# Kernel tuning notes

Measured on AMD Instinct MI355X. Metric: run time of the kernel, lower is better.

Reference implementation:

```python
import jax, jax.numpy as jnp
import numpy as np

N_PIXELS = 1024 * 1024      # flattened image W*H
N_CLASSES = 100             # logit channels / label vocabulary
N_SEGMENTS = 30             # superpixel_regions


def setup_inputs() -> dict:
    key = jax.random.key(0)
    k1, k2, k3 = jax.random.split(key, 3)
    output = jax.random.normal(k1, (N_PIXELS, N_CLASSES), dtype=jnp.float32)
    target = jax.random.randint(k2, (N_PIXELS,), 0, N_CLASSES, dtype=jnp.int64)
    seg_ids = jax.random.randint(k3, (N_PIXELS,), 0, N_SEGMENTS, dtype=jnp.int32)
    return {"output": output, "target": target, "seg_ids": seg_ids}


def reference(output, target, seg_ids):
    # --- per-superpixel histogram mode-voting relabel ---
    # counts[s, c] = number of pixels in superpixel s currently labeled c.
    counts = jnp.zeros((N_SEGMENTS, N_CLASSES), dtype=jnp.int32)
    counts = counts.at[seg_ids, target].add(1)
    # np.argmax over hist of np.unique-sorted labels == smallest class id among ties,
    # which jnp.argmax over the dense class axis reproduces exactly.
    mode = jnp.argmax(counts, axis=1)              # [S]
    relabeled = mode[seg_ids].astype(target.dtype)  # [N]

    # --- CrossEntropyLoss(output, target): mean NLL of log-softmax ---
    logp = jax.nn.log_softmax(output, axis=-1)                       # [N, C]
    nll = -jnp.take_along_axis(logp, target[:, None], axis=-1)[:, 0]  # [N]
    loss = jnp.mean(nll)
    return loss, relabeled
```

## Files before the change

### kernel.cpp

```cpp
#include <hip/hip_runtime.h>
#include <math.h>

#define NCLASS 100
#define NSEG 30

__global__ __launch_bounds__(256) void ce_hist_kernel(
    const float* __restrict__ logits,
    const int*   __restrict__ target,
    const int*   __restrict__ seg,
    int N,
    int*    __restrict__ g_counts,
    double* __restrict__ g_loss)
{
    __shared__ int    lds_hist[NSEG * NCLASS];
    __shared__ double lds_loss[4];

    for (int i = threadIdx.x; i < NSEG * NCLASS; i += blockDim.x) lds_hist[i] = 0;
    __syncthreads();

    const int lane          = threadIdx.x & 63;
    const int wave          = threadIdx.x >> 6;
    const int sub           = lane & 3;
    const int q             = lane >> 2;
    const int wavesPerBlock = blockDim.x >> 6;
    const int gwave         = blockIdx.x * wavesPerBlock + wave;
    const int totWaves      = gridDim.x * wavesPerBlock;
    const int ngroups       = (N + 15) >> 4;

    double acc = 0.0;

    for (int grp = gwave; grp < ngroups; grp += totWaves) {
        const int  row   = grp * 16 + q;
        const bool valid = (row < N);

        const float NEG = -INFINITY;
        float4 f0, f1, f2, f3, f4, f5, f6;
        f0 = f1 = f2 = f3 = f4 = f5 = f6 = make_float4(NEG, NEG, NEG, NEG);
        int t = 0, s = 0;
        float xt = 0.0f;

        if (valid) {
            const float4* r4 = (const float4*)(logits + (size_t)row * NCLASS);
            f0 = r4[sub +  0];
            f1 = r4[sub +  4];
            f2 = r4[sub +  8];
            f3 = r4[sub + 12];
            f4 = r4[sub + 16];
            f5 = r4[sub + 20];
            if (sub == 0) f6 = r4[24];
            t = target[row];
            s = seg[row];
            xt = logits[(size_t)row * NCLASS + t];
        }

        float e = 0.0f;
        e += __expf(f0.x) + __expf(f0.y) + __expf(f0.z) + __expf(f0.w);
        e += __expf(f1.x) + __expf(f1.y) + __expf(f1.z) + __expf(f1.w);
        e += __expf(f2.x) + __expf(f2.y) + __expf(f2.z) + __expf(f2.w);
        e += __expf(f3.x) + __expf(f3.y) + __expf(f3.z) + __expf(f3.w);
        e += __expf(f4.x) + __expf(f4.y) + __expf(f4.z) + __expf(f4.w);
        e += __expf(f5.x) + __expf(f5.y) + __expf(f5.z) + __expf(f5.w);
        e += __expf(f6.x) + __expf(f6.y) + __expf(f6.z) + __expf(f6.w);
        e += __shfl_xor(e, 1);
        e += __shfl_xor(e, 2);

        if (valid && sub == 0) {
            float lse = __logf(e);
            acc += (double)(lse - xt);
            atomicAdd(&lds_hist[s * NCLASS + t], 1);
        }
    }

    #pragma unroll
    for (int off = 32; off; off >>= 1) acc += __shfl_xor(acc, off);
    if (lane == 0) lds_loss[wave] = acc;
    __syncthreads();

    if (threadIdx.x == 0) {
        double b = 0.0;
        for (int w = 0; w < wavesPerBlock; ++w) b += lds_loss[w];
        atomicAdd(g_loss, b);
    }
    for (int i = threadIdx.x; i < NSEG * NCLASS; i += blockDim.x) {
        int c = lds_hist[i];
        if (c) atomicAdd(&g_counts[i], c);
    }
}

__global__ void finalize_kernel(
    const int* __restrict__ g_counts,
    const double* __restrict__ g_loss,
    int N,
    int* __restrict__ g_mode,
    float* __restrict__ out_loss)
{
    const int t = threadIdx.x;
    const int s = t >> 3;
    const int j = t & 7;
    if (s < NSEG) {
        int bestKey = -1;
        #pragma unroll
        for (int c = j; c < NCLASS; c += 8) {
            int v = g_counts[s * NCLASS + c];
            int key = (v << 7) | (127 - c);
            bestKey = max(bestKey, key);
        }
        bestKey = max(bestKey, __shfl_xor(bestKey, 1));
        bestKey = max(bestKey, __shfl_xor(bestKey, 2));
        bestKey = max(bestKey, __shfl_xor(bestKey, 4));
        if (j == 0) g_mode[s] = 127 - (bestKey & 127);
    }
    if (t == 0) out_loss[0] = (float)(g_loss[0] / (double)N);
}

__global__ __launch_bounds__(256) void relabel_kernel(
    const int* __restrict__ seg,
    const int* __restrict__ g_mode,
    float* __restrict__ out,
    int N)
{
    __shared__ float mode_f[NSEG];
    for (int i = threadIdx.x; i < NSEG; i += blockDim.x)
        mode_f[i] = (float)g_mode[i];
    __syncthreads();

    int idx    = blockIdx.x * blockDim.x + threadIdx.x;
    int stride = gridDim.x * blockDim.x;
    for (int i = idx; i < N; i += stride)
        out[i] = mode_f[seg[i]];
}

extern "C" void kernel_launch(void* const* d_in, const int* in_sizes, int n_in,
                              void* d_out, int out_size, void* d_ws, size_t ws_size,
                              hipStream_t stream)
{
    const float* logits = (const float*)d_in[0];
    const int*   target = (const int*)d_in[1];
    const int*   seg    = (const int*)d_in[2];
    float* out = (float*)d_out;

    const int N = in_sizes[1];

    double* g_loss   = (double*)d_ws;
    int*    g_counts = (int*)((char*)d_ws + 16);
    int*    g_mode   = (int*)((char*)d_ws + 16 + NSEG * NCLASS * sizeof(int));

    hipMemsetAsync(d_ws, 0, 16 + NSEG * NCLASS * sizeof(int), stream);

    ce_hist_kernel<<<2048, 256, 0, stream>>>(logits, target, seg, N, g_counts, g_loss);
    finalize_kernel<<<1, 256, 0, stream>>>(g_counts, g_loss, N, g_mode, out);
    relabel_kernel<<<1024, 256, 0, stream>>>(seg, g_mode, out + 1, N);
}
```

Baseline: 117.0 us.

## Coalesce logits loads across 16-row group and reduce partial exps through LDS

Each wave now reads its 16-row group (400 float4s) as one contiguous block with lane-strided float4 loads, instead of per-row strided loads. Per-float4 exp sums are written to a per-wave LDS buffer and regathered per row before the shuffle reduction. The tail-row guard is dropped, so N must be a multiple of 16, and the main grid is halved. The aim is better global memory coalescing, paid for with extra LDS traffic and no intra-wave barrier around the LDS buffer reuse.

```diff
diff --git a/kernel.cpp b/kernel.cpp
--- a/kernel.cpp
+++ b/kernel.cpp
@@ -3,6 +3,13 @@
 
 #define NCLASS 100
 #define NSEG 30
+#define F4_PER_ROW 25
+#define ROWS_PER_GRP 16
+#define F4_PER_GRP (F4_PER_ROW * ROWS_PER_GRP)
+
+__device__ __forceinline__ float e4(float4 v) {
+    return __expf(v.x) + __expf(v.y) + __expf(v.z) + __expf(v.w);
+}
 
 __global__ __launch_bounds__(256) void ce_hist_kernel(
     const float* __restrict__ logits,
@@ -13,67 +20,66 @@
     double* __restrict__ g_loss)
 {
     __shared__ int    lds_hist[NSEG * NCLASS];
+    __shared__ float  part[4][F4_PER_GRP];
     __shared__ double lds_loss[4];
 
     for (int i = threadIdx.x; i < NSEG * NCLASS; i += blockDim.x) lds_hist[i] = 0;
     __syncthreads();
 
     const int lane          = threadIdx.x & 63;
-    const int wave          = threadIdx.x >> 6;
+    const int wv            = threadIdx.x >> 6;
     const int sub           = lane & 3;
     const int q             = lane >> 2;
     const int wavesPerBlock = blockDim.x >> 6;
-    const int gwave         = blockIdx.x * wavesPerBlock + wave;
+    const int gwave         = blockIdx.x * wavesPerBlock + wv;
     const int totWaves      = gridDim.x * wavesPerBlock;
-    const int ngroups       = (N + 15) >> 4;
+    const int ngroups       = N >> 4;
 
     double acc = 0.0;
 
     for (int grp = gwave; grp < ngroups; grp += totWaves) {
-        const int  row   = grp * 16 + q;
-        const bool valid = (row < N);
+        const int row = grp * ROWS_PER_GRP + q;
 
-        const float NEG = -INFINITY;
-        float4 f0, f1, f2, f3, f4, f5, f6;
-        f0 = f1 = f2 = f3 = f4 = f5 = f6 = make_float4(NEG, NEG, NEG, NEG);
-        int t = 0, s = 0;
-        float xt = 0.0f;
+        const int t = target[row];
+        const int s = seg[row];
 
-        if (valid) {
-            const float4* r4 = (const float4*)(logits + (size_t)row * NCLASS);
-            f0 = r4[sub +  0];
-            f1 = r4[sub +  4];
-            f2 = r4[sub +  8];
-            f3 = r4[sub + 12];
-            f4 = r4[sub + 16];
-            f5 = r4[sub + 20];
-            if (sub == 0) f6 = r4[24];
-            t = target[row];
-            s = seg[row];
-            xt = logits[(size_t)row * NCLASS + t];
+        const float4* g4 = (const float4*)logits + (size_t)grp * F4_PER_GRP;
+        float4 f0 = g4[lane        ];
+        float4 f1 = g4[lane + 64   ];
+        float4 f2 = g4[lane + 128  ];
+        float4 f3 = g4[lane + 192  ];
+        float4 f4v= g4[lane + 256  ];
+        float4 f5 = g4[lane + 320  ];
+
+        part[wv][lane      ] = e4(f0);
+        part[wv][lane + 64 ] = e4(f1);
+        part[wv][lane + 128] = e4(f2);
+        part[wv][lane + 192] = e4(f3);
+        part[wv][lane + 256] = e4(f4v);
+        part[wv][lane + 320] = e4(f5);
+        if (lane < 16) {
+            float4 f6 = g4[lane + 384];
+            part[wv][lane + 384] = e4(f6);
         }
 
-        float e = 0.0f;
-        e += __expf(f0.x) + __expf(f0.y) + __expf(f0.z) + __expf(f0.w);
-        e += __expf(f1.x) + __expf(f1.y) + __expf(f1.z) + __expf(f1.w);
-        e += __expf(f2.x) + __expf(f2.y) + __expf(f2.z) + __expf(f2.w);
-        e += __expf(f3.x) + __expf(f3.y) + __expf(f3.z) + __expf(f3.w);
-        e += __expf(f4.x) + __expf(f4.y) + __expf(f4.z) + __expf(f4.w);
-        e += __expf(f5.x) + __expf(f5.y) + __expf(f5.z) + __expf(f5.w);
-        e += __expf(f6.x) + __expf(f6.y) + __expf(f6.z) + __expf(f6.w);
+        const int base = F4_PER_ROW * q + sub;
+        float e = part[wv][base     ] + part[wv][base + 4 ] + part[wv][base + 8 ]
+                + part[wv][base + 12] + part[wv][base + 16] + part[wv][base + 20];
+        if (sub == 0) e += part[wv][F4_PER_ROW * q + 24];
         e += __shfl_xor(e, 1);
         e += __shfl_xor(e, 2);
 
-        if (valid && sub == 0) {
-            float lse = __logf(e);
-            acc += (double)(lse - xt);
+        const float xt = logits[(size_t)row * NCLASS + t];
+
+        if (sub == 0) {
+            acc += (double)(__logf(e) - xt);
             atomicAdd(&lds_hist[s * NCLASS + t], 1);
         }
     }
 
     #pragma unroll
     for (int off = 32; off; off >>= 1) acc += __shfl_xor(acc, off);
-    if (lane == 0) lds_loss[wave] = acc;
+    if (lane == 0) lds_loss[wv] = acc;
     __syncthreads();
 
     if (threadIdx.x == 0) {
@@ -147,7 +153,7 @@
 
     hipMemsetAsync(d_ws, 0, 16 + NSEG * NCLASS * sizeof(int), stream);
 
-    ce_hist_kernel<<<2048, 256, 0, stream>>>(logits, target, seg, N, g_counts, g_loss);
+    ce_hist_kernel<<<1024, 256, 0, stream>>>(logits, target, seg, N, g_counts, g_loss);
     finalize_kernel<<<1, 256, 0, stream>>>(g_counts, g_loss, N, g_mode, out);
     relabel_kernel<<<1024, 256, 0, stream>>>(seg, g_mode, out + 1, N);
 }
```

Measured after the change: 108.7 us. 1.08x faster.
